# Kernel optimization log

Hardware: AMD Instinct MI355X
Metric: run time of the kernel (lower is better)

Reference implementation:

```python
import jax, jax.numpy as jnp
import numpy as np

ALPHA = 32.0
EPS = 1e-8
NEG_SLOPE = 0.01  # torch F.leaky_relu default


def setup_inputs() -> dict:
    key = jax.random.key(0)
    k_x, k_h, k_a, k_b, k_c, k_d = jax.random.split(key, 6)
    B, S, D_IN, D_OUT, R = 4, 4096, 4096, 4096, 16
    std = 1.0 / np.sqrt(R)
    return {
        "x": jax.random.normal(k_x, (B, S, D_IN), dtype=jnp.float32),
        "h_t": jax.random.uniform(k_h, (B, S, R), dtype=jnp.float32),
        "W_a": jax.random.normal(k_a, (D_IN, R), dtype=jnp.float32) * std,
        "W_b": jax.random.normal(k_b, (R, D_OUT), dtype=jnp.float32) * std,
        "W_c": jax.random.normal(k_c, (R, R), dtype=jnp.float32) * std,
        "W_d": jax.random.normal(k_d, (R, R), dtype=jnp.float32) * std,
    }


def reference(x, h_t, W_a, W_b, W_c, W_d):
    # x: [B,S,in_dim]; h_t: [B,S,rank] (recurrent state already shape-matched)
    new_x = jnp.einsum("bsd,dr->bsr", x, W_a)            # [B,S,R]
    h_t1 = h_t @ W_c + new_x @ W_d + h_t                  # [B,S,R]
    # min-max normalization over the rank axis (dim=2)
    min_val = jnp.min(h_t1, axis=2, keepdims=True)
    max_val = jnp.max(h_t1, axis=2, keepdims=True)
    h_norm = (h_t1 - min_val) / (max_val - min_val + EPS)
    # dropout in eval mode (identity); leaky_relu with torch default slope
    act = jnp.where(h_norm >= 0, h_norm, NEG_SLOPE * h_norm)
    y = ALPHA * jnp.einsum("bsr,ro->bso", new_x + act, W_b)  # [B,S,out_dim]
    return y
```

## Files before the change

kernel.cpp:

```cpp
#include <hip/hip_runtime.h>

#define ALPHA_F 32.0f
#define EPS_F 1e-8f
#define NEG_SLOPE_F 0.01f

#define D_IN 4096
#define D_OUT 4096
#define RNK 16
#define N_ROWS 16384
#define ROWS_PER_BLOCK 16
#define THREADS 256

__global__ __launch_bounds__(THREADS) void ssm_lora_fused(
    const float* __restrict__ x,
    const float* __restrict__ h_t,
    const float* __restrict__ Wa,
    const float* __restrict__ Wb,
    const float* __restrict__ Wc,
    const float* __restrict__ Wd,
    float* __restrict__ y)
{
    __shared__ float red[4][16][68];
    __shared__ float lds_nx[16][16];
    __shared__ float lds_u[16][16];

    const int tid  = threadIdx.x;
    const int lane = tid & 63;
    const int w    = tid >> 6;
    const long row0 = (long)blockIdx.x * ROWS_PER_BLOCK;
    const int wr0  = w * 4;

    float acc[4][16];
    #pragma unroll
    for (int rr = 0; rr < 4; ++rr)
        #pragma unroll
        for (int r = 0; r < 16; ++r) acc[rr][r] = 0.0f;

    const float4* x4 = (const float4*)x;
    const long xbase = (row0 + wr0) * (D_IN / 4);

    for (int k = 0; k < 16; ++k) {
        const int p = lane + (k << 6);
        float4 xv[4];
        #pragma unroll
        for (int rr = 0; rr < 4; ++rr)
            xv[rr] = x4[xbase + (long)rr * (D_IN / 4) + p];

        #pragma unroll
        for (int dd = 0; dd < 4; ++dd) {
            const float4* war = (const float4*)(Wa + ((size_t)(4 * p + dd) << 4));
            const float4 w0 = war[0], w1 = war[1], w2 = war[2], w3 = war[3];
            #pragma unroll
            for (int rr = 0; rr < 4; ++rr) {
                const float xs = ((const float*)&xv[rr])[dd];
                acc[rr][0]  += xs * w0.x;  acc[rr][1]  += xs * w0.y;
                acc[rr][2]  += xs * w0.z;  acc[rr][3]  += xs * w0.w;
                acc[rr][4]  += xs * w1.x;  acc[rr][5]  += xs * w1.y;
                acc[rr][6]  += xs * w1.z;  acc[rr][7]  += xs * w1.w;
                acc[rr][8]  += xs * w2.x;  acc[rr][9]  += xs * w2.y;
                acc[rr][10] += xs * w2.z;  acc[rr][11] += xs * w2.w;
                acc[rr][12] += xs * w3.x;  acc[rr][13] += xs * w3.y;
                acc[rr][14] += xs * w3.z;  acc[rr][15] += xs * w3.w;
            }
        }
    }

    #pragma unroll
    for (int rr = 0; rr < 4; ++rr)
        #pragma unroll
        for (int r = 0; r < 16; ++r) {
            float v = acc[rr][r];
            v += __shfl_xor(v, 1, 64);
            v += __shfl_xor(v, 2, 64);
            acc[rr][r] = v;
        }
    if ((lane & 3) == 0) {
        const int li = lane >> 2;
        #pragma unroll
        for (int rr = 0; rr < 4; ++rr)
            #pragma unroll
            for (int r = 0; r < 16; ++r)
                red[w][li][rr * 16 + r] = acc[rr][r];
    }
    __syncthreads();

    {
        const int row  = tid >> 4;
        const int r    = tid & 15;
        const int w2   = tid >> 6;
        const int slot = tid & 63;
        float s = 0.0f;
        #pragma unroll
        for (int i = 0; i < 16; ++i) s += red[w2][i][slot];
        lds_nx[row][r] = s;
        __syncthreads();

        const float* hrow = h_t + (row0 + row) * RNK;
        float h1 = hrow[r];
        #pragma unroll
        for (int j = 0; j < 16; ++j)
            h1 += hrow[j] * Wc[j * 16 + r] + lds_nx[row][j] * Wd[j * 16 + r];

        float mn = h1, mx = h1;
        #pragma unroll
        for (int m = 1; m <= 8; m <<= 1) {
            mn = fminf(mn, __shfl_xor(mn, m, 64));
            mx = fmaxf(mx, __shfl_xor(mx, m, 64));
        }
        const float hn = (h1 - mn) / (mx - mn + EPS_F);
        const float a  = (hn >= 0.0f) ? hn : NEG_SLOPE_F * hn;
        lds_u[row][r] = ALPHA_F * (s + a);
    }
    __syncthreads();

    float4 uu[4][4];
    #pragma unroll
    for (int rr = 0; rr < 4; ++rr)
        #pragma unroll
        for (int j = 0; j < 4; ++j)
            uu[rr][j] = ((const float4*)lds_u[wr0 + rr])[j];

    const float4* Wb4 = (const float4*)Wb;
    float4* y4 = (float4*)y;
    const long ybase = (row0 + wr0) * (D_OUT / 4);

    for (int k = 0; k < 16; ++k) {
        const int p = lane + (k << 6);
        float4 wb[16];
        #pragma unroll
        for (int r2 = 0; r2 < 16; ++r2) wb[r2] = Wb4[(size_t)r2 * 1024 + p];
        #pragma unroll
        for (int rr = 0; rr < 4; ++rr) {
            float4 o; o.x = 0.0f; o.y = 0.0f; o.z = 0.0f; o.w = 0.0f;
            #pragma unroll
            for (int r2 = 0; r2 < 16; ++r2) {
                const float us = ((const float*)&uu[rr][0])[r2];
                o.x += us * wb[r2].x;
                o.y += us * wb[r2].y;
                o.z += us * wb[r2].z;
                o.w += us * wb[r2].w;
            }
            y4[ybase + (long)rr * (D_OUT / 4) + p] = o;
        }
    }
}

extern "C" void kernel_launch(void* const* d_in, const int* in_sizes, int n_in,
                              void* d_out, int out_size, void* d_ws, size_t ws_size,
                              hipStream_t stream) {
    const float* x   = (const float*)d_in[0];
    const float* h_t = (const float*)d_in[1];
    const float* Wa  = (const float*)d_in[2];
    const float* Wb  = (const float*)d_in[3];
    const float* Wc  = (const float*)d_in[4];
    const float* Wd  = (const float*)d_in[5];
    float* y = (float*)d_out;

    dim3 grid(N_ROWS / ROWS_PER_BLOCK);
    dim3 block(THREADS);
    ssm_lora_fused<<<grid, block, 0, stream>>>(x, h_t, Wa, Wb, Wc, Wd, y);
}
```

Baseline: 655.1 us.

## Transpose W_a for coalesced loads, prefetch x, and split W_b loads

Adds a small pre-kernel that transposes W_a into the workspace, so the first GEMM reads coalesced float4 rows per rank instead of strided 64-byte chunks per lane. The x loads are software-prefetched one iteration ahead, and the W_b loop loads eight rows at a time to cut register pressure, together with a launch_bounds occupancy hint. This costs an extra kernel launch and workspace traffic, and the dot-product form changes the accumulation order.

New measurement: 1.062 ms. 1.62x slower.

```diff
diff --git a/kernel.cpp b/kernel.cpp
--- a/kernel.cpp
+++ b/kernel.cpp
@@ -11,10 +11,19 @@
 #define ROWS_PER_BLOCK 16
 #define THREADS 256
 
-__global__ __launch_bounds__(THREADS) void ssm_lora_fused(
+__global__ __launch_bounds__(256) void transpose_wa(
+    const float* __restrict__ Wa, float* __restrict__ WaT)
+{
+    const int idx = blockIdx.x * 256 + threadIdx.x;
+    const int r = idx >> 12;
+    const int d = idx & 4095;
+    WaT[idx] = Wa[d * RNK + r];
+}
+
+__global__ __launch_bounds__(THREADS, 4) void ssm_lora_fused(
     const float* __restrict__ x,
     const float* __restrict__ h_t,
-    const float* __restrict__ Wa,
+    const float* __restrict__ WaT,
     const float* __restrict__ Wb,
     const float* __restrict__ Wc,
     const float* __restrict__ Wd,
@@ -36,31 +45,33 @@
         #pragma unroll
         for (int r = 0; r < 16; ++r) acc[rr][r] = 0.0f;
 
-    const float4* x4 = (const float4*)x;
+    const float4* x4   = (const float4*)x;
+    const float4* WaT4 = (const float4*)WaT;
     const long xbase = (row0 + wr0) * (D_IN / 4);
 
+    float4 xv[4];
+    #pragma unroll
+    for (int rr = 0; rr < 4; ++rr)
+        xv[rr] = x4[xbase + (long)rr * (D_IN / 4) + lane];
+
     for (int k = 0; k < 16; ++k) {
+        float4 xc[4];
+        #pragma unroll
+        for (int rr = 0; rr < 4; ++rr) xc[rr] = xv[rr];
+        if (k < 15) {
+            const int pn = lane + ((k + 1) << 6);
+            #pragma unroll
+            for (int rr = 0; rr < 4; ++rr)
+                xv[rr] = x4[xbase + (long)rr * (D_IN / 4) + pn];
+        }
         const int p = lane + (k << 6);
-        float4 xv[4];
         #pragma unroll
-        for (int rr = 0; rr < 4; ++rr)
-            xv[rr] = x4[xbase + (long)rr * (D_IN / 4) + p];
-
-        #pragma unroll
-        for (int dd = 0; dd < 4; ++dd) {
-            const float4* war = (const float4*)(Wa + ((size_t)(4 * p + dd) << 4));
-            const float4 w0 = war[0], w1 = war[1], w2 = war[2], w3 = war[3];
+        for (int r = 0; r < 16; ++r) {
+            const float4 w4 = WaT4[(size_t)r * (D_IN / 4) + p];
             #pragma unroll
             for (int rr = 0; rr < 4; ++rr) {
-                const float xs = ((const float*)&xv[rr])[dd];
-                acc[rr][0]  += xs * w0.x;  acc[rr][1]  += xs * w0.y;
-                acc[rr][2]  += xs * w0.z;  acc[rr][3]  += xs * w0.w;
-                acc[rr][4]  += xs * w1.x;  acc[rr][5]  += xs * w1.y;
-                acc[rr][6]  += xs * w1.z;  acc[rr][7]  += xs * w1.w;
-                acc[rr][8]  += xs * w2.x;  acc[rr][9]  += xs * w2.y;
-                acc[rr][10] += xs * w2.z;  acc[rr][11] += xs * w2.w;
-                acc[rr][12] += xs * w3.x;  acc[rr][13] += xs * w3.y;
-                acc[rr][14] += xs * w3.z;  acc[rr][15] += xs * w3.w;
+                acc[rr][r] += xc[rr].x * w4.x + xc[rr].y * w4.y
+                            + xc[rr].z * w4.z + xc[rr].w * w4.w;
             }
         }
     }
@@ -126,22 +137,31 @@
 
     for (int k = 0; k < 16; ++k) {
         const int p = lane + (k << 6);
-        float4 wb[16];
+        float4 o[4];
         #pragma unroll
-        for (int r2 = 0; r2 < 16; ++r2) wb[r2] = Wb4[(size_t)r2 * 1024 + p];
+        for (int rr = 0; rr < 4; ++rr) { o[rr].x = o[rr].y = o[rr].z = o[rr].w = 0.0f; }
         #pragma unroll
-        for (int rr = 0; rr < 4; ++rr) {
-            float4 o; o.x = 0.0f; o.y = 0.0f; o.z = 0.0f; o.w = 0.0f;
+        for (int half = 0; half < 2; ++half) {
+            float4 wb[8];
             #pragma unroll
-            for (int r2 = 0; r2 < 16; ++r2) {
-                const float us = ((const float*)&uu[rr][0])[r2];
-                o.x += us * wb[r2].x;
-                o.y += us * wb[r2].y;
-                o.z += us * wb[r2].z;
-                o.w += us * wb[r2].w;
+            for (int j = 0; j < 8; ++j)
+                wb[j] = Wb4[(size_t)(half * 8 + j) * (D_OUT / 4) + p];
+            #pragma unroll
+            for (int rr = 0; rr < 4; ++rr) {
+                #pragma unroll
+                for (int j = 0; j < 8; ++j) {
+                    const int r2 = half * 8 + j;
+                    const float us = ((const float*)&uu[rr][0])[r2];
+                    o[rr].x += us * wb[j].x;
+                    o[rr].y += us * wb[j].y;
+                    o[rr].z += us * wb[j].z;
+                    o[rr].w += us * wb[j].w;
+                }
             }
-            y4[ybase + (long)rr * (D_OUT / 4) + p] = o;
         }
+        #pragma unroll
+        for (int rr = 0; rr < 4; ++rr)
+            y4[ybase + (long)rr * (D_OUT / 4) + p] = o[rr];
     }
 }
 
@@ -154,9 +174,10 @@
     const float* Wb  = (const float*)d_in[3];
     const float* Wc  = (const float*)d_in[4];
     const float* Wd  = (const float*)d_in[5];
-    float* y = (float*)d_out;
+    float* y   = (float*)d_out;
+    float* WaT = (float*)d_ws;
 
-    dim3 grid(N_ROWS / ROWS_PER_BLOCK);
-    dim3 block(THREADS);
-    ssm_lora_fused<<<grid, block, 0, stream>>>(x, h_t, Wa, Wb, Wc, Wd, y);
+    transpose_wa<<<dim3((D_IN * RNK) / 256), dim3(256), 0, stream>>>(Wa, WaT);
+    ssm_lora_fused<<<dim3(N_ROWS / ROWS_PER_BLOCK), dim3(THREADS), 0, stream>>>(
+        x, h_t, WaT, Wb, Wc, Wd, y);
 }
```
